# Kernel tuning notes

Measured on AMD Instinct MI355X. Metric: run time of the kernel, lower is better.

## Reference

```python
import jax, jax.numpy as jnp
import numpy as np

N = 100000   # nodes
E = 3200000  # edges
CY = 128     # channels_y (signal length per node)
HID = 10     # hidden_channels
H = 2        # heads
C = 10       # out channels per head
BN_EPS = 1e-5


def _glorot(k, shape):
    lim = float(np.sqrt(6.0 / (shape[0] + shape[1])))
    return jax.random.uniform(k, shape, jnp.float32, -lim, lim)


def setup_inputs() -> dict:
    key = jax.random.key(0)
    ks = jax.random.split(key, 16)
    p = {}
    p["signal"] = jax.random.normal(ks[0], (N, CY), jnp.float32)
    p["edge_index"] = jax.random.randint(ks[1], (2, E), 0, N)
    p["edge_weight"] = jax.random.uniform(ks[2], (E,), jnp.float32)
    p["mask"] = jax.random.bernoulli(ks[3], 0.3, (N,))
    # mlp_in: Linear(CY,512) -> BatchNorm -> ReLU -> Linear(512,HID) (PyG MLP, plain_last)
    p["W1"] = _glorot(ks[4], (CY, 512)); p["b1"] = jnp.zeros((512,), jnp.float32)
    p["gamma"] = jnp.ones((512,), jnp.float32); p["beta"] = jnp.zeros((512,), jnp.float32)
    p["W2"] = _glorot(ks[5], (512, HID)); p["b2"] = jnp.zeros((HID,), jnp.float32)
    # GATv2Conv(HID, HID, heads=2, edge_dim=1, concat=True)
    p["Wl"] = _glorot(ks[6], (HID, H * C)); p["bl"] = jnp.zeros((H * C,), jnp.float32)
    p["Wr"] = _glorot(ks[7], (HID, H * C)); p["br"] = jnp.zeros((H * C,), jnp.float32)
    p["We"] = _glorot(ks[8], (1, H * C))              # lin_edge, no bias
    p["att"] = _glorot(ks[9], (H, C))                 # attention vector per head
    p["gat_bias"] = jnp.zeros((H * C,), jnp.float32)
    # mlp_out: MLP([20,512]) single layer, plain_last -> just Linear (dropout off in eval)
    p["W3"] = _glorot(ks[10], (H * C, 512)); p["b3"] = jnp.zeros((512,), jnp.float32)
    # out_linear: Linear(512, CY)
    p["W4"] = _glorot(ks[11], (512, CY)); p["b4"] = jnp.zeros((CY,), jnp.float32)
    return p


def _forward(signal, edge_index, edge_weight, mask,
             W1, b1, gamma, beta, W2, b2,
             Wl, bl, Wr, br, We, att, gat_bias,
             W3, b3, W4, b4):
    # node masking: (signal.T * ~mask).T
    x = signal * (~mask)[:, None].astype(signal.dtype)
    # mlp_in (eval mode: BN with running mean=0, var=1)
    x = x @ W1 + b1
    x = x * (gamma / jnp.sqrt(jnp.asarray(1.0 + BN_EPS, x.dtype))) + beta
    x = jax.nn.relu(x)
    x = x @ W2 + b2                                   # [N, HID]
    # GATv2Conv
    src, dst = edge_index[0], edge_index[1]
    xl = (x @ Wl + bl).reshape(N, H, C)               # source transform
    xr = (x @ Wr + br).reshape(N, H, C)               # target transform
    ea = (edge_weight[:, None] @ We).reshape(E, H, C)  # edge feature transform
    e = jax.nn.leaky_relu(xl[src] + xr[dst] + ea, 0.2)  # [E,H,C]
    alpha = jnp.einsum('ehc,hc->eh', e, att)          # [E,H]
    # segment softmax over incoming edges of each dst node
    m = jax.ops.segment_max(alpha, dst, num_segments=N)
    ex = jnp.exp(alpha - m[dst])
    den = jax.ops.segment_sum(ex, dst, num_segments=N)
    a = ex / (den[dst] + 1e-16)                       # [E,H]
    out = jax.ops.segment_sum(xl[src] * a[:, :, None], dst, num_segments=N)
    out = out.reshape(N, H * C) + gat_bias            # concat heads + bias
    # mlp_out (single plain-last layer) + out_linear
    out = out @ W3 + b3
    out = out @ W4 + b4
    return out


def reference(signal, edge_index, edge_weight, mask,
              W1, b1, gamma, beta, W2, b2,
              Wl, bl, Wr, br, We, att, gat_bias,
              W3, b3, W4, b4):
    return _forward(signal, edge_index, edge_weight, mask,
                    W1, b1, gamma, beta, W2, b2,
                    Wl, bl, Wr, br, We, att, gat_bias,
                    W3, b3, W4, b4)
```

## Files before the change

### kernel.cpp

```cpp
#include <hip/hip_runtime.h>
#include <hip/hip_bf16.h>

constexpr int NN = 100000;
constexpr int NE = 3200000;
constexpr int CYC = 128;
constexpr int NB = 1563;
constexpr int EBLK = 256;
constexpr int ECHUNK = NE / EBLK;
constexpr int MSCAN = NB * EBLK;
constexpr int CAP = 2432;
constexpr int NBLK_A = (NN + 63) / 64;

#define OFF_W1T    0u
#define OFF_W2T    131072u
#define OFF_B1E    147456u
#define OFF_SMALL  149504u
#define OFF_W34    151808u
#define OFF_B34    162048u
#define OFF_FLAGS  162560u
#define OFF_XLB    163840u
#define OFF_XR     6563840u
#define OFF_NS     14563840u
#define OFF_GH     14965248u
#define OFF_BB     16565760u
#define OFF_BS     16572160u
#define OFF_BIN    16573184u

#define SF_WLR 0
#define SF_BLR 400
#define SF_ATT 440
#define SF_WE  460
#define SF_GB  480
#define SF_B2  500

typedef __attribute__((ext_vector_type(8))) short bf16x8;
typedef __attribute__((ext_vector_type(4))) float f32x4;

__device__ __forceinline__ float bfu(unsigned short x) {
  return __uint_as_float(((unsigned)x) << 16);
}
__device__ __forceinline__ short f2bf(float f) {
  __hip_bfloat16 h = __float2bfloat16(f);
  return *reinterpret_cast<short*>(&h);
}
__device__ __forceinline__ float LD(const void* p, long i, int f32f) {
  return f32f ? ((const float*)p)[i] : bfu(((const unsigned short*)p)[i]);
}

__global__ __launch_bounds__(256) void kPrep(
    const void* __restrict__ W1, const void* __restrict__ b1,
    const void* __restrict__ gamma, const void* __restrict__ beta,
    const void* __restrict__ W2, const void* __restrict__ b2,
    const void* __restrict__ Wl, const void* __restrict__ bl,
    const void* __restrict__ Wr, const void* __restrict__ br,
    const void* __restrict__ We, const void* __restrict__ att,
    const void* __restrict__ gbias, const void* __restrict__ W3,
    const void* __restrict__ b3, const void* __restrict__ W4,
    const void* __restrict__ b4, const void* __restrict__ mask,
    int* __restrict__ flags,
    short* __restrict__ W1T, float* __restrict__ b1eff, short* __restrict__ W2T,
    float* __restrict__ smallf, float* __restrict__ W34, float* __restrict__ b34)
{
  __shared__ int sfl[2];
  int t = threadIdx.x;
  if (t < 64) {
    const unsigned short* W1u = (const unsigned short*)W1;
    const unsigned* masku = (const unsigned*)mask;
    int big = 0;
#pragma unroll
    for (int k = 0; k < 8; k++) {
      unsigned e = (W1u[t * 8 + k] >> 7) & 0xFF;
      if (e >= 170) big++;
    }
    int byt = 0;
#pragma unroll
    for (int k = 0; k < 4; k++) if (masku[t * 4 + k] & ~1u) byt = 1;
#pragma unroll
    for (int o = 1; o < 64; o <<= 1) {
      big += __shfl_xor(big, o);
      byt |= __shfl_xor(byt, o);
    }
    if (t == 0) {
      sfl[0] = (big >= 4) ? 1 : 0;
      sfl[1] = byt;
      if (blockIdx.x == 0) { flags[0] = sfl[0]; flags[1] = byt; }
    }
  }
  __syncthreads();
  const int f32f = sfl[0];

  int tid = blockIdx.x * 256 + t;
  const float rs = 0.999995000037f;
  if (tid < 65536) {
    int j = tid >> 7, k = tid & 127;
    float s = LD(gamma, j, f32f) * rs;
    W1T[j * 128 + k] = f2bf(LD(W1, k * 512 + j, f32f) * s);
    if (k == 0) b1eff[j] = LD(b1, j, f32f) * s + LD(beta, j, f32f);
  } else if (tid < 73728) {
    int i = tid - 65536;
    int c = i >> 9, k = i & 511;
    W2T[c * 512 + k] = (c < 10) ? f2bf(LD(W2, k * 10 + c, f32f)) : (short)0;
  } else if (tid < 114688) {
    int i = tid - 73728;
    int o = i >> 4, k0 = i & 15;
    int j = o >> 7, tt = o & 127;
    float acc = 0.f;
    for (int k = k0; k < 512; k += 16)
      acc += LD(W3, j * 512 + k, f32f) * LD(W4, k * 128 + tt, f32f);
#pragma unroll
    for (int o2 = 1; o2 < 16; o2 <<= 1) acc += __shfl_xor(acc, o2);
    if (k0 == 0) W34[o] = acc;
  } else if (tid < 116736) {
    int i = tid - 114688;
    int tt = i >> 4, k0 = i & 15;
    float acc = 0.f;
    for (int k = k0; k < 512; k += 16)
      acc += LD(b3, k, f32f) * LD(W4, k * 128 + tt, f32f);
#pragma unroll
    for (int o2 = 1; o2 < 16; o2 <<= 1) acc += __shfl_xor(acc, o2);
    if (k0 == 0) b34[tt] = acc + LD(b4, tt, f32f);
  } else if (tid < 117252) {
    int i = tid - 116736;
    if (i < 400) {
      int c = i / 40, o = i % 40;
      smallf[SF_WLR + i] = (o < 20) ? LD(Wl, c * 20 + o, f32f) : LD(Wr, c * 20 + (o - 20), f32f);
    } else if (i < 440) {
      int o = i - 400;
      smallf[SF_BLR + o] = (o < 20) ? LD(bl, o, f32f) : LD(br, o - 20, f32f);
    } else if (i < 460) {
      smallf[SF_ATT + (i - 440)] = LD(att, i - 440, f32f);
    } else if (i < 480) {
      smallf[SF_WE + (i - 460)] = LD(We, i - 460, f32f);
    } else if (i < 500) {
      smallf[SF_GB + (i - 480)] = LD(gbias, i - 480, f32f);
    } else {
      int c = i - 500;
      smallf[SF_B2 + c] = (c < 10) ? LD(b2, c, f32f) : 0.f;
    }
  }
}

__global__ __launch_bounds__(256, 2) void kA(
    const void* __restrict__ sig, const void* __restrict__ mask,
    const short* __restrict__ W1T, const float* __restrict__ b1eff,
    const short* __restrict__ W2T, const float* __restrict__ smallf,
    const int* __restrict__ flags,
    unsigned short* __restrict__ xlb, float* __restrict__ xr)
{
  __shared__ __align__(16) char sR1[17408];
  __shared__ short sH[4][32 * 136];
  __shared__ float sb1[512];
  __shared__ float sxh[64][12];
  __shared__ float sWlr[400];
  __shared__ float sblr[40];
  __shared__ float sb2[16];

  short (*sA)[136]        = (short (*)[136])sR1;
  float (*sxhp)[64][17]   = (float (*)[64][17])sR1;
  float (*sxlr)[40]       = (float (*)[40])sR1;

  const int f32f = flags[0];
  const int mk8  = flags[1];
  int t = threadIdx.x;
  int w = t >> 6, l = t & 63;
  int lrow = l & 15, quad = l >> 4;
  int row0 = blockIdx.x * 64;

  for (int i = t; i < 512; i += 256) sb1[i] = b1eff[i];
  for (int i = t; i < 400; i += 256) sWlr[i] = smallf[SF_WLR + i];
  if (t < 40) sblr[t] = smallf[SF_BLR + t];
  if (t < 16) sb2[t] = smallf[SF_B2 + t];

  bf16x8 zz = {0, 0, 0, 0, 0, 0, 0, 0};
#pragma unroll
  for (int k = 0; k < 4; k++) {
    int idx = t + k * 256;
    int row = idx >> 4, seg = idx & 15;
    int gr = row0 + row;
    int grc = gr < NN ? gr : NN - 1;
    bool mbit = mk8 ? (((const unsigned char*)mask)[grc] != 0)
                    : (((const int*)mask)[grc] != 0);
    bf16x8 v;
    if (mbit) {
      v = zz;
    } else if (f32f) {
      const float4* Sf = (const float4*)((const float*)sig + (size_t)grc * CYC) + seg * 2;
      float4 x0 = Sf[0], x1 = Sf[1];
      v[0] = f2bf(x0.x); v[1] = f2bf(x0.y); v[2] = f2bf(x0.z); v[3] = f2bf(x0.w);
      v[4] = f2bf(x1.x); v[5] = f2bf(x1.y); v[6] = f2bf(x1.z); v[7] = f2bf(x1.w);
    } else {
      v = ((const bf16x8*)((const unsigned short*)sig + (size_t)grc * CYC))[seg];
    }
    *(bf16x8*)&sA[row][seg * 8] = v;
  }
  __syncthreads();

  float bcol[8];
#pragma unroll
  for (int ct = 0; ct < 8; ct++) bcol[ct] = sb1[w * 128 + ct * 16 + lrow];

  f32x4 acc[4][8];
#pragma unroll
  for (int rf = 0; rf < 4; rf++)
#pragma unroll
    for (int ct = 0; ct < 8; ct++) acc[rf][ct] = (f32x4){0.f, 0.f, 0.f, 0.f};

  const bf16x8* Bp = (const bf16x8*)W1T;
  int bvbase = w * 2048 + lrow * 16 + quad;
#pragma unroll
  for (int kt = 0; kt < 4; kt++) {
    bf16x8 a0 = *(const bf16x8*)&sA[lrow][kt * 32 + quad * 8];
    bf16x8 a1 = *(const bf16x8*)&sA[16 + lrow][kt * 32 + quad * 8];
    bf16x8 a2f = *(const bf16x8*)&sA[32 + lrow][kt * 32 + quad * 8];
    bf16x8 a3 = *(const bf16x8*)&sA[48 + lrow][kt * 32 + quad * 8];
#pragma unroll
    for (int ct = 0; ct < 8; ct++) {
      bf16x8 bv = Bp[bvbase + ct * 256 + kt * 4];
      acc[0][ct] = __builtin_amdgcn_mfma_f32_16x16x32_bf16(a0, bv, acc[0][ct], 0, 0, 0);
      acc[1][ct] = __builtin_amdgcn_mfma_f32_16x16x32_bf16(a1, bv, acc[1][ct], 0, 0, 0);
      acc[2][ct] = __builtin_amdgcn_mfma_f32_16x16x32_bf16(a2f, bv, acc[2][ct], 0, 0, 0);
      acc[3][ct] = __builtin_amdgcn_mfma_f32_16x16x32_bf16(a3, bv, acc[3][ct], 0, 0, 0);
    }
  }
  __syncthreads();

  const bf16x8* B2p = (const bf16x8*)W2T;
  bf16x8 b2v[4];
#pragma unroll
  for (int kt2 = 0; kt2 < 4; kt2++) b2v[kt2] = B2p[lrow * 64 + w * 16 + kt2 * 4 + quad];

  short* hb = &sH[w][0];
#pragma unroll
  for (int hf = 0; hf < 2; hf++) {
#pragma unroll
    for (int rr = 0; rr < 2; rr++) {
      int rf = hf * 2 + rr;
#pragma unroll
      for (int ct = 0; ct < 8; ct++) {
        float bb = bcol[ct];
#pragma unroll
        for (int r = 0; r < 4; r++) {
          float vv = fmaxf(acc[rf][ct][r] + bb, 0.f);
          hb[(rr * 16 + quad * 4 + r) * 136 + ct * 16 + lrow] = f2bf(vv);
        }
      }
    }
    asm volatile("s_waitcnt lgkmcnt(0)" ::: "memory");

    f32x4 a2[2];
    a2[0] = (f32x4){0.f, 0.f, 0.f, 0.f};
    a2[1] = (f32x4){0.f, 0.f, 0.f, 0.f};
#pragma unroll
    for (int kt2 = 0; kt2 < 4; kt2++) {
      bf16x8 x0 = *(const bf16x8*)&hb[lrow * 136 + kt2 * 32 + quad * 8];
      bf16x8 x1 = *(const bf16x8*)&hb[(16 + lrow) * 136 + kt2 * 32 + quad * 8];
      a2[0] = __builtin_amdgcn_mfma_f32_16x16x32_bf16(x0, b2v[kt2], a2[0], 0, 0, 0);
      a2[1] = __builtin_amdgcn_mfma_f32_16x16x32_bf16(x1, b2v[kt2], a2[1], 0, 0, 0);
    }
#pragma unroll
    for (int f = 0; f < 2; f++)
#pragma unroll
      for (int r = 0; r < 4; r++)
        sxhp[w][hf * 32 + f * 16 + quad * 4 + r][lrow] = a2[f][r];
  }
  __syncthreads();

  for (int i = t; i < 640; i += 256) {
    int row = i / 10, c = i - row * 10;
    sxh[row][c] = sxhp[0][row][c] + sxhp[1][row][c] + sxhp[2][row][c] + sxhp[3][row][c] + sb2[c];
  }
  __syncthreads();

  for (int i = t; i < 2560; i += 256) {
    int row = i / 40, o = i - row * 40;
    float v = sblr[o];
#pragma unroll
    for (int c = 0; c < 10; c++) v += sxh[row][c] * sWlr[c * 40 + o];
    sxlr[row][o] = v;
  }
  __syncthreads();

  int nrows = NN - row0; if (nrows > 64) nrows = 64;
  unsigned* xlb32 = (unsigned*)xlb;
#pragma unroll
  for (int k = 0; k < 4; k++) {
    int i = t + k * 256;
    int row = i >> 4, p = i & 15;
    if (row < nrows) {
      int s0 = 2 * p, s1 = 2 * p + 1;
      float lo = (s0 < 10) ? sxlr[row][s0] : (s0 >= 16 && s0 < 26) ? sxlr[row][s0 - 6] : 0.f;
      float hi = (s1 < 10) ? sxlr[row][s1] : (s1 >= 16 && s1 < 26) ? sxlr[row][s1 - 6] : 0.f;
      unsigned u = (unsigned)(unsigned short)f2bf(lo) |
                   ((unsigned)(unsigned short)f2bf(hi) << 16);
      xlb32[(size_t)(row0 + row) * 16 + p] = u;
    }
  }
#pragma unroll
  for (int k = 0; k < 5; k++) {
    int i = t + k * 256;
    int row = i / 20, c = i - row * 20;
    if (row < nrows) xr[(size_t)(row0 + row) * 20 + c] = sxlr[row][20 + c];
  }
}

__global__ __launch_bounds__(256) void kB1(const int* __restrict__ ei,
                                           int* __restrict__ gh) {
  __shared__ int h[NB];
  int t = threadIdx.x, blk = blockIdx.x;
  for (int i = t; i < NB; i += 256) h[i] = 0;
  __syncthreads();
  const int* dst = ei + NE;
  int base = blk * ECHUNK, bend = base + ECHUNK;
  for (int i = base + t; i < bend; i += 256)
    atomicAdd(&h[dst[i] >> 6], 1);
  __syncthreads();
  for (int i = t; i < NB; i += 256) gh[i * EBLK + blk] = h[i];
}

__global__ __launch_bounds__(256) void kS1(const int* __restrict__ in,
                                           int* __restrict__ outx,
                                           int* __restrict__ bsum, int nelem) {
  __shared__ int sS[256];
  int t = threadIdx.x;
  int base = blockIdx.x * 2048 + t * 8;
  int d[8], tsum = 0;
#pragma unroll
  for (int k = 0; k < 8; k++) {
    d[k] = (base + k < nelem) ? in[base + k] : 0;
    tsum += d[k];
  }
  sS[t] = tsum;
  __syncthreads();
  for (int o = 1; o < 256; o <<= 1) {
    int v = (t >= o) ? sS[t - o] : 0;
    __syncthreads();
    sS[t] += v;
    __syncthreads();
  }
  int run = sS[t] - tsum;
#pragma unroll
  for (int k = 0; k < 8; k++) {
    if (base + k < nelem) outx[base + k] = run;
    run += d[k];
  }
  if (t == 255) bsum[blockIdx.x] = sS[255];
}

__global__ __launch_bounds__(256) void kS2(int* __restrict__ bsum, int nb) {
  __shared__ int sS[256];
  int t = threadIdx.x;
  int v = (t < nb) ? bsum[t] : 0;
  sS[t] = v;
  __syncthreads();
  for (int o = 1; o < 256; o <<= 1) {
    int u = (t >= o) ? sS[t - o] : 0;
    __syncthreads();
    sS[t] += u;
    __syncthreads();
  }
  if (t < nb) bsum[t] = sS[t] - v;
}

__global__ __launch_bounds__(256) void kS3(int* __restrict__ gh,
                                           const int* __restrict__ bsum,
                                           int* __restrict__ bb) {
  int i = blockIdx.x * 256 + threadIdx.x;
  int v = gh[i] + bsum[i >> 11];
  gh[i] = v;
  if ((i & 255) == 0) bb[i >> 8] = v;
  if (i == 0) bb[NB] = NE;
}

__global__ __launch_bounds__(256) void kB3(const int* __restrict__ ei,
                                           const void* __restrict__ ew,
                                           const int* __restrict__ flags,
                                           const int* __restrict__ gh,
                                           int2* __restrict__ binned) {
  __shared__ int cur[NB];
  const int f32f = flags[0];
  int t = threadIdx.x, blk = blockIdx.x;
  for (int i = t; i < NB; i += 256) cur[i] = gh[i * EBLK + blk];
  __syncthreads();
  int base = blk * ECHUNK, bend = base + ECHUNK;
  for (int i = base + t; i < bend; i += 256) {
    int s = ei[i], d = ei[NE + i];
    float w = LD(ew, i, f32f);
    int b = d >> 6;
    int pos = atomicAdd(&cur[b], 1);
    binned[pos] = make_int2(s | ((d & 63) << 17), __float_as_int(w));
  }
}

__global__ __launch_bounds__(256) void kSort(const int* __restrict__ bb,
                                             int2* __restrict__ binned,
                                             int* __restrict__ nstart) {
  __shared__ int2 sRaw[CAP];
  __shared__ int sCnt[64], sPre[64], sCur[64];
  int t = threadIdx.x, b = blockIdx.x;
  int base = bb[b], end = bb[b + 1];
  int ne = end - base;
  if (ne > CAP) ne = CAP;
  if (t < 64) sCnt[t] = 0;
  __syncthreads();
  for (int i = t; i < ne; i += 256) {
    int2 e = binned[base + i];
    sRaw[i] = e;
    atomicAdd(&sCnt[(unsigned)e.x >> 17], 1);
  }
  __syncthreads();
  if (t < 64) sPre[t] = sCnt[t];
  __syncthreads();
  for (int o = 1; o < 64; o <<= 1) {
    int v = 0;
    if (t < 64 && t >= o) v = sPre[t - o];
    __syncthreads();
    if (t < 64) sPre[t] += v;
    __syncthreads();
  }
  if (t < 64) {
    int ex = sPre[t] - sCnt[t];
    sCur[t] = ex;
    nstart[b * 64 + t] = base + ex;
  }
  if (t == 63 && b == NB - 1) nstart[NB * 64] = base + sPre[63];
  __syncthreads();
  for (int i = t; i < ne; i += 256) {
    int2 e = sRaw[i];
    int dl = (unsigned)e.x >> 17;
    int pos = atomicAdd(&sCur[dl], 1);
    binned[base + pos] = make_int2(e.x & 0x1FFFF, e.y);
  }
}

__global__ __launch_bounds__(512) void kAgg(
    const int* __restrict__ nstart, const int2* __restrict__ binned,
    const unsigned short* __restrict__ xlb, const float* __restrict__ xr,
    const float* __restrict__ smallf, const float* __restrict__ W34,
    const float* __restrict__ b34, const int* __restrict__ flags,
    void* __restrict__ out)
{
  __shared__ float sXr[64 * 20];
  __shared__ float sW[2560];
  __shared__ float sb[128];
  __shared__ int   sStart[65];
  __shared__ float sAtt[20], sWe[20], sGb[20];

  const int f32f = flags[0];
  int t = threadIdx.x, b = blockIdx.x;
  int node0 = b * 64;

  for (int i = t; i < 2560; i += 512) sW[i] = W34[i];
  for (int i = t; i < 1280; i += 512) {
    int gi = node0 * 20 + i;
    sXr[i] = (gi < NN * 20) ? xr[gi] : 0.f;
  }
  if (t < 128) sb[t] = b34[t];
  if (t < 65) sStart[t] = nstart[node0 + t];
  if (t < 20) { sAtt[t] = smallf[SF_ATT + t]; sWe[t] = smallf[SF_WE + t]; sGb[t] = smallf[SF_GB + t]; }
  __syncthreads();

  int n = t >> 3, sub = t & 7, head = sub >> 2, part = sub & 3;
  float xrw[10], attw[10], wew[10];
#pragma unroll
  for (int c = 0; c < 10; c++) {
    xrw[c]  = sXr[n * 20 + head * 10 + c];
    attw[c] = sAtt[head * 10 + c];
    wew[c]  = sWe[head * 10 + c];
  }
  float acc[10];
#pragma unroll
  for (int c = 0; c < 10; c++) acc[c] = 0.f;
  float den = 0.f;
  int s0 = sStart[n], s1 = sStart[n + 1];

  int i = s0 + part;
  int2 e; uint4 q; unsigned q4;
  if (i < s1) {
    e = binned[i];
    const unsigned short* p = xlb + (size_t)e.x * 32 + head * 16;
    q = *(const uint4*)p;
    q4 = *(const unsigned*)(p + 8);
  }
  while (i < s1) {
    int j = i + 4;
    int2 en; uint4 qn; unsigned qn4;
    if (j < s1) {
      en = binned[j];
      const unsigned short* pn = xlb + (size_t)en.x * 32 + head * 16;
      qn = *(const uint4*)pn;
      qn4 = *(const unsigned*)(pn + 8);
    }
    float vl[10];
    unsigned qq[5] = {q.x, q.y, q.z, q.w, q4};
#pragma unroll
    for (int k = 0; k < 5; k++) {
      vl[2 * k]     = __uint_as_float(qq[k] << 16);
      vl[2 * k + 1] = __uint_as_float(qq[k] & 0xffff0000u);
    }
    float ww = __int_as_float(e.y);
    float a = 0.f;
#pragma unroll
    for (int c = 0; c < 10; c++) {
      float v = vl[c] + xrw[c] + ww * wew[c];
      v = fmaxf(v, 0.2f * v);
      a += v * attw[c];
    }
    float pp = __expf(a);
    den += pp;
#pragma unroll
    for (int c = 0; c < 10; c++) acc[c] += pp * vl[c];
    e = en; q = qn; q4 = qn4; i = j;
  }
  den += __shfl_xor(den, 1);
  den += __shfl_xor(den, 2);
#pragma unroll
  for (int c = 0; c < 10; c++) {
    acc[c] += __shfl_xor(acc[c], 1);
    acc[c] += __shfl_xor(acc[c], 2);
  }

  __syncthreads();
  if (part == 0) {
    float inv = 1.f / (den + 1e-16f);
#pragma unroll
    for (int c = 0; c < 10; c++)
      sXr[n * 20 + head * 10 + c] = acc[c] * inv + sGb[head * 10 + c];
  }
  __syncthreads();

  int col = t & 127, grp = t >> 7;
  for (int n2 = grp; n2 < 64; n2 += 4) {
    int gn = node0 + n2;
    if (gn >= NN) break;
    float v = sb[col];
    const float* g = &sXr[n2 * 20];
#pragma unroll
    for (int c = 0; c < 20; c++) v += g[c] * sW[c * 128 + col];
    if (f32f) ((float*)out)[(size_t)gn * 128 + col] = v;
    else ((unsigned short*)out)[(size_t)gn * 128 + col] = (unsigned short)f2bf(v);
  }
}

extern "C" void kernel_launch(void* const* d_in, const int* in_sizes, int n_in,
                              void* d_out, int out_size, void* d_ws, size_t ws_size,
                              hipStream_t stream) {
  (void)in_sizes; (void)n_in; (void)out_size; (void)ws_size;
  const void* sig  = d_in[0];
  const int*  ei   = (const int*)d_in[1];
  const void* ew   = d_in[2];
  const void* mask = d_in[3];
  const void* W1   = d_in[4];
  const void* b1   = d_in[5];
  const void* gam  = d_in[6];
  const void* bet  = d_in[7];
  const void* W2   = d_in[8];
  const void* b2   = d_in[9];
  const void* Wl   = d_in[10];
  const void* bl   = d_in[11];
  const void* Wr   = d_in[12];
  const void* br   = d_in[13];
  const void* We   = d_in[14];
  const void* att  = d_in[15];
  const void* gb   = d_in[16];
  const void* W3   = d_in[17];
  const void* b3   = d_in[18];
  const void* W4   = d_in[19];
  const void* b4   = d_in[20];

  char* ws = (char*)d_ws;
  short* W1T    = (short*)(ws + OFF_W1T);
  short* W2T    = (short*)(ws + OFF_W2T);
  float* b1eff  = (float*)(ws + OFF_B1E);
  float* smallf = (float*)(ws + OFF_SMALL);
  float* W34    = (float*)(ws + OFF_W34);
  float* b34    = (float*)(ws + OFF_B34);
  int*   flags  = (int*)(ws + OFF_FLAGS);
  unsigned short* xlb = (unsigned short*)(ws + OFF_XLB);
  float* xr     = (float*)(ws + OFF_XR);
  int*   nstart = (int*)(ws + OFF_NS);
  int*   gh     = (int*)(ws + OFF_GH);
  int*   bb     = (int*)(ws + OFF_BB);
  int*   bsum   = (int*)(ws + OFF_BS);
  int2*  bincsr = (int2*)(ws + OFF_BIN);

  kPrep<<<459, 256, 0, stream>>>(W1, b1, gam, bet, W2, b2, Wl, bl, Wr, br, We, att,
                                 gb, W3, b3, W4, b4, mask, flags,
                                 W1T, b1eff, W2T, smallf, W34, b34);
  kA<<<NBLK_A, 256, 0, stream>>>(sig, mask, W1T, b1eff, W2T, smallf, flags, xlb, xr);
  kB1<<<EBLK, 256, 0, stream>>>(ei, gh);
  kS1<<<(MSCAN + 2047) / 2048, 256, 0, stream>>>(gh, gh, bsum, MSCAN);
  kS2<<<1, 256, 0, stream>>>(bsum, (MSCAN + 2047) / 2048);
  kS3<<<NB, 256, 0, stream>>>(gh, bsum, bb);
  kB3<<<EBLK, 256, 0, stream>>>(ei, ew, flags, gh, bincsr);
  kSort<<<NB, 256, 0, stream>>>(bb, bincsr, nstart);
  kAgg<<<NB, 512, 0, stream>>>(nstart, bincsr, xlb, xr, smallf, W34, b34, flags, d_out);
}
```

Baseline: 422.3 us.

## Fuse per-bin counting sort into aggregation kernel using shared-memory edge list

Removes the separate kSort launch and the global nstart array. The aggregation kernel now counts and scatters its own bin's edges by local destination into a shared-memory buffer, then reads edge entries from LDS instead of global memory. This drops one kernel launch and a global write/read pass over the binned edges. In exchange it raises LDS usage per block, which may lower occupancy, and it adds a serial sort phase before aggregation. Edges beyond CAP are dropped, the same truncation the old kSort applied.

```diff
diff --git a/kernel.cpp b/kernel.cpp
--- a/kernel.cpp
+++ b/kernel.cpp
@@ -20,7 +20,6 @@
 #define OFF_FLAGS  162560u
 #define OFF_XLB    163840u
 #define OFF_XR     6563840u
-#define OFF_NS     14563840u
 #define OFF_GH     14965248u
 #define OFF_BB     16565760u
 #define OFF_BS     16572160u
@@ -391,23 +390,41 @@
   }
 }
 
-__global__ __launch_bounds__(256) void kSort(const int* __restrict__ bb,
-                                             int2* __restrict__ binned,
-                                             int* __restrict__ nstart) {
-  __shared__ int2 sRaw[CAP];
-  __shared__ int sCnt[64], sPre[64], sCur[64];
+__global__ __launch_bounds__(512) void kAgg(
+    const int* __restrict__ bb, const int2* __restrict__ binned,
+    const unsigned short* __restrict__ xlb, const float* __restrict__ xr,
+    const float* __restrict__ smallf, const float* __restrict__ W34,
+    const float* __restrict__ b34, const int* __restrict__ flags,
+    void* __restrict__ out)
+{
+  __shared__ int2  sES[CAP];
+  __shared__ float sXr[64 * 20];
+  __shared__ float sW[2560];
+  __shared__ float sb[128];
+  __shared__ int   sCnt[64], sPre[64], sStart[64], sCur[64];
+  __shared__ float sAtt[20], sWe[20], sGb[20];
+
+  const int f32f = flags[0];
   int t = threadIdx.x, b = blockIdx.x;
+  int node0 = b * 64;
+
+  for (int i = t; i < 2560; i += 512) sW[i] = W34[i];
+  for (int i = t; i < 1280; i += 512) {
+    int gi = node0 * 20 + i;
+    sXr[i] = (gi < NN * 20) ? xr[gi] : 0.f;
+  }
+  if (t < 128) sb[t] = b34[t];
+  if (t < 64) sCnt[t] = 0;
+  if (t < 20) { sAtt[t] = smallf[SF_ATT + t]; sWe[t] = smallf[SF_WE + t]; sGb[t] = smallf[SF_GB + t]; }
+  __syncthreads();
+
   int base = bb[b], end = bb[b + 1];
   int ne = end - base;
-  if (ne > CAP) ne = CAP;
-  if (t < 64) sCnt[t] = 0;
-  __syncthreads();
-  for (int i = t; i < ne; i += 256) {
-    int2 e = binned[base + i];
-    sRaw[i] = e;
-    atomicAdd(&sCnt[(unsigned)e.x >> 17], 1);
-  }
-  __syncthreads();
+
+  for (int i = t; i < ne; i += 512)
+    atomicAdd(&sCnt[(unsigned)binned[base + i].x >> 17], 1);
+  __syncthreads();
+
   if (t < 64) sPre[t] = sCnt[t];
   __syncthreads();
   for (int o = 1; o < 64; o <<= 1) {
@@ -419,44 +436,17 @@
   }
   if (t < 64) {
     int ex = sPre[t] - sCnt[t];
+    sStart[t] = ex;
     sCur[t] = ex;
-    nstart[b * 64 + t] = base + ex;
-  }
-  if (t == 63 && b == NB - 1) nstart[NB * 64] = base + sPre[63];
-  __syncthreads();
-  for (int i = t; i < ne; i += 256) {
-    int2 e = sRaw[i];
+  }
+  __syncthreads();
+
+  for (int i = t; i < ne; i += 512) {
+    int2 e = binned[base + i];
     int dl = (unsigned)e.x >> 17;
     int pos = atomicAdd(&sCur[dl], 1);
-    binned[base + pos] = make_int2(e.x & 0x1FFFF, e.y);
-  }
-}
-
-__global__ __launch_bounds__(512) void kAgg(
-    const int* __restrict__ nstart, const int2* __restrict__ binned,
-    const unsigned short* __restrict__ xlb, const float* __restrict__ xr,
-    const float* __restrict__ smallf, const float* __restrict__ W34,
-    const float* __restrict__ b34, const int* __restrict__ flags,
-    void* __restrict__ out)
-{
-  __shared__ float sXr[64 * 20];
-  __shared__ float sW[2560];
-  __shared__ float sb[128];
-  __shared__ int   sStart[65];
-  __shared__ float sAtt[20], sWe[20], sGb[20];
-
-  const int f32f = flags[0];
-  int t = threadIdx.x, b = blockIdx.x;
-  int node0 = b * 64;
-
-  for (int i = t; i < 2560; i += 512) sW[i] = W34[i];
-  for (int i = t; i < 1280; i += 512) {
-    int gi = node0 * 20 + i;
-    sXr[i] = (gi < NN * 20) ? xr[gi] : 0.f;
-  }
-  if (t < 128) sb[t] = b34[t];
-  if (t < 65) sStart[t] = nstart[node0 + t];
-  if (t < 20) { sAtt[t] = smallf[SF_ATT + t]; sWe[t] = smallf[SF_WE + t]; sGb[t] = smallf[SF_GB + t]; }
+    if (pos < CAP) sES[pos] = make_int2(e.x & 0x1FFFF, e.y);
+  }
   __syncthreads();
 
   int n = t >> 3, sub = t & 7, head = sub >> 2, part = sub & 3;
@@ -471,12 +461,14 @@
 #pragma unroll
   for (int c = 0; c < 10; c++) acc[c] = 0.f;
   float den = 0.f;
-  int s0 = sStart[n], s1 = sStart[n + 1];
+  int s0 = sStart[n];
+  int s1 = s0 + sCnt[n];
+  if (s1 > CAP) s1 = CAP;
 
   int i = s0 + part;
   int2 e; uint4 q; unsigned q4;
   if (i < s1) {
-    e = binned[i];
+    e = sES[i];
     const unsigned short* p = xlb + (size_t)e.x * 32 + head * 16;
     q = *(const uint4*)p;
     q4 = *(const unsigned*)(p + 8);
@@ -485,7 +477,7 @@
     int j = i + 4;
     int2 en; uint4 qn; unsigned qn4;
     if (j < s1) {
-      en = binned[j];
+      en = sES[j];
       const unsigned short* pn = xlb + (size_t)en.x * 32 + head * 16;
       qn = *(const uint4*)pn;
       qn4 = *(const unsigned*)(pn + 8);
@@ -577,7 +569,6 @@
   int*   flags  = (int*)(ws + OFF_FLAGS);
   unsigned short* xlb = (unsigned short*)(ws + OFF_XLB);
   float* xr     = (float*)(ws + OFF_XR);
-  int*   nstart = (int*)(ws + OFF_NS);
   int*   gh     = (int*)(ws + OFF_GH);
   int*   bb     = (int*)(ws + OFF_BB);
   int*   bsum   = (int*)(ws + OFF_BS);
@@ -592,6 +583,5 @@
   kS2<<<1, 256, 0, stream>>>(bsum, (MSCAN + 2047) / 2048);
   kS3<<<NB, 256, 0, stream>>>(gh, bsum, bb);
   kB3<<<EBLK, 256, 0, stream>>>(ei, ew, flags, gh, bincsr);
-  kSort<<<NB, 256, 0, stream>>>(bb, bincsr, nstart);
-  kAgg<<<NB, 512, 0, stream>>>(nstart, bincsr, xlb, xr, smallf, W34, b34, flags, d_out);
-}
+  kAgg<<<NB, 512, 0, stream>>>(bb, bincsr, xlb, xr, smallf, W34, b34, flags, d_out);
+}
```

Result: faster. 403.1 us (-4.5%).
